# Kernel tuning notes

Hardware: AMD Instinct MI355X
Metric: run time of the kernel (lower is better)

## Reference

```python
import jax, jax.numpy as jnp
import numpy as np

NI, ND, NH = 64, 64, 4
NB, NLOC, NNEI = 4, 2048, 64


def setup_inputs() -> dict:
    key = jax.random.key(0)
    ks = jax.random.split(key, 7)
    g1 = jax.random.normal(ks[0], (NB, NLOC, NI), dtype=jnp.float32)
    gg1 = jax.random.normal(ks[1], (NB, NLOC, NNEI, NI), dtype=jnp.float32)
    nlist_mask = jax.random.randint(ks[2], (NB, NLOC, NNEI), 0, 2).astype(bool)
    # torch Linear weight (out, in); store transposed for x @ W
    Wq = jax.random.normal(ks[3], (NI, ND * NH), dtype=jnp.float32) * (1.0 / np.sqrt(NI))
    Wkv = jax.random.normal(ks[4], (NI, (ND + NI) * NH), dtype=jnp.float32) * (1.0 / np.sqrt(NI))
    Wh = jax.random.normal(ks[5], (NI * NH, NI), dtype=jnp.float32) * (1.0 / np.sqrt(NI * NH))
    bh = jax.random.normal(ks[6], (NI,), dtype=jnp.float32) * 0.01
    return {"g1": g1, "gg1": gg1, "nlist_mask": nlist_mask,
            "Wq": Wq, "Wkv": Wkv, "Wh": Wh, "bh": bh}


def reference(g1, gg1, nlist_mask, Wq, Wkv, Wh, bh):
    nb, nloc, nnei = nlist_mask.shape
    ni, nd, nh = NI, ND, NH
    # q: (nb, nloc, nh, nd)
    q = (g1 @ Wq).reshape(nb, nloc, nd, nh).transpose(0, 1, 3, 2)
    # kv: (nb, nloc, nnei, nd, 2*nh) -> (nb, nloc, 2*nh, nnei, nd); valid since ni == nd
    kv = (gg1 @ Wkv).reshape(nb, nloc, nnei, nd, 2 * nh).transpose(0, 1, 4, 2, 3)
    k = kv[:, :, :nh]          # (nb, nloc, nh, nnei, nd)
    v = kv[:, :, nh:2 * nh]    # (nb, nloc, nh, nnei, nd)
    attnw = jnp.einsum('blhd,blhjd->blhj', q, k) / np.sqrt(nd).astype(np.float32)
    m = nlist_mask[:, :, None, :]  # (nb, nloc, 1, nnei)
    attnw = jnp.where(m, attnw, -jnp.inf)
    attnw = jax.nn.softmax(attnw, axis=-1)
    attnw = jnp.where(m, attnw, 0.0)
    ret = jnp.einsum('blhj,blhjd->blhd', attnw, v).reshape(nb, nloc, nh * ni)
    return ret @ Wh + bh
```

## Files before the change

### kernel.cpp

```cpp
#include <hip/hip_runtime.h>
#include <hip/hip_fp16.h>
#include <math.h>

#define NATOM 8192

namespace {

typedef _Float16 half8 __attribute__((ext_vector_type(8)));
typedef _Float16 half2t __attribute__((ext_vector_type(2)));
typedef float f32x4 __attribute__((ext_vector_type(4)));

constexpr int VB_STRIDE = 260;

__global__ void pack_weights(const float* __restrict__ Wkv,
                             const float* __restrict__ Wq,
                             const float* __restrict__ Wh,
                             _Float16* __restrict__ out) {
  int tid = blockIdx.x * 256 + threadIdx.x;
  if (tid < 32768) {
    int i = tid >> 9, c = tid & 511;
    int ks = i >> 5, jj = i & 7, lq = (i >> 3) & 3;
    int ct = c >> 4, lr = c & 15;
    int l = lq * 16 + lr;
    out[(((ct * 2 + ks) * 64) + l) * 8 + jj] = (_Float16)Wkv[i * 512 + c];
  } else if (tid < 49152) {
    int idx = tid - 32768;
    int i = idx >> 8, c = idx & 255;
    out[32768 + c * 64 + i] = (_Float16)Wq[i * 256 + c];
  } else {
    int idx = tid - 49152;
    int k = idx >> 6, c = idx & 63;
    out[49152 + c * 256 + k] = (_Float16)Wh[k * 64 + c];
  }
}

__device__ __forceinline__ float dot8(half8 a, half8 b, float acc) {
  acc = __builtin_amdgcn_fdot2((half2t){a[0], a[1]}, (half2t){b[0], b[1]}, acc, false);
  acc = __builtin_amdgcn_fdot2((half2t){a[2], a[3]}, (half2t){b[2], b[3]}, acc, false);
  acc = __builtin_amdgcn_fdot2((half2t){a[4], a[5]}, (half2t){b[4], b[5]}, acc, false);
  acc = __builtin_amdgcn_fdot2((half2t){a[6], a[7]}, (half2t){b[6], b[7]}, acc, false);
  return acc;
}

__global__ __launch_bounds__(256, 4)
void local_atten_kernel(const float* __restrict__ g1,
                        const float* __restrict__ gg1,
                        const int* __restrict__ mask,
                        const _Float16* __restrict__ wpack,
                        const float* __restrict__ bh,
                        float* __restrict__ out) {
  __shared__ __align__(16) __half vraw[64 * VB_STRIDE];
  __shared__ __align__(16) __half g1h[64];
  __shared__ __align__(16) unsigned char blob[3072];
  __shared__ __align__(8) __half aws2[64][4];
  __shared__ __align__(16) __half rets[256];

  float* qs = reinterpret_cast<float*>(blob);
  __half (*sred)[4][64] = reinterpret_cast<__half(*)[4][64]>(blob + 1024);
  __half (*redbuf2)[64][4] = reinterpret_cast<__half(*)[64][4]>(blob);
  float (*redbuf)[64] = reinterpret_cast<float(*)[64]>(blob + 2048);

  const _Float16* wkvp = wpack;
  const _Float16* wqp  = wpack + 32768;
  const _Float16* whp  = wpack + 49152;

  const int t = threadIdx.x;
  const int lane = t & 63;
  const int wave = t >> 6;
  const int lq = lane >> 4;
  const int lr = lane & 15;
  const int atom = blockIdx.x;

  __half* gs = vraw;
  auto vbuf = reinterpret_cast<__half(*)[VB_STRIDE]>(vraw);

  const int mreg = mask[(size_t)atom * 64 + lane];
  const float bhv = bh[lane];
  if (t < 64) g1h[t] = __float2half(g1[(size_t)atom * 64 + t]);

  {
    const float4* src = reinterpret_cast<const float4*>(gg1 + (size_t)atom * 4096);
#pragma unroll
    for (int r = 0; r < 4; ++r) {
      int idx4 = t + 256 * r;
      int j = idx4 >> 4;
      int i4 = (idx4 & 15) << 2;
      float4 v = src[idx4];
      __half2 h01 = __floats2half2_rn(v.x, v.y);
      __half2 h23 = __floats2half2_rn(v.z, v.w);
      int g = i4 >> 3;
      int addr = j * 64 + ((g ^ (j & 7)) << 3) + (i4 & 7);
      union { __half2 h[2]; uint2 u; } pk;
      pk.h[0] = h01; pk.h[1] = h23;
      *reinterpret_cast<uint2*>(&gs[addr]) = pk.u;
    }
  }
  __syncthreads();

  half8 bfrag[4][2];
#pragma unroll
  for (int jt = 0; jt < 4; ++jt) {
#pragma unroll
    for (int ks = 0; ks < 2; ++ks) {
      int j = jt * 16 + lr;
      int g = ks * 4 + lq;
      bfrag[jt][ks] =
          *reinterpret_cast<const half8*>(&gs[j * 64 + ((g ^ (j & 7)) << 3)]);
    }
  }

  const half8* ap_base = reinterpret_cast<const half8*>(wkvp);
  half8 a0 = ap_base[(wave * 4) * 128 + lane];
  half8 a1 = ap_base[(wave * 4) * 128 + 64 + lane];

  {
    float qacc = 0.f;
    const half8* wrow = reinterpret_cast<const half8*>(wqp + t * 64);
    const half8* grow = reinterpret_cast<const half8*>(&g1h[0]);
#pragma unroll
    for (int ks = 0; ks < 8; ++ks) qacc = dot8(wrow[ks], grow[ks], qacc);
    qs[t] = qacc;
  }
  __syncthreads();

  float sacc[4][4];
#pragma unroll
  for (int jt = 0; jt < 4; ++jt)
#pragma unroll
    for (int h = 0; h < 4; ++h) sacc[jt][h] = 0.f;

  const bool isv = (lq & 1);
#pragma unroll
  for (int it = 0; it < 8; ++it) {
    const int ct = ((it >> 2) << 4) + wave * 4 + (it & 3);
    const int d = ct * 2 + (lq >> 1);

    half8 na0 = a0, na1 = a1;
    if (it < 7) {
      const int nit = it + 1;
      const int nct = ((nit >> 2) << 4) + wave * 4 + (nit & 3);
      na0 = ap_base[nct * 128 + lane];
      na1 = ap_base[nct * 128 + 64 + lane];
    }

    f32x4 accs[4];
#pragma unroll
    for (int jt = 0; jt < 4; ++jt) {
      f32x4 acc = {0.f, 0.f, 0.f, 0.f};
      acc = __builtin_amdgcn_mfma_f32_16x16x32_f16(a0, bfrag[jt][0], acc, 0, 0, 0);
      acc = __builtin_amdgcn_mfma_f32_16x16x32_f16(a1, bfrag[jt][1], acc, 0, 0, 0);
      accs[jt] = acc;
    }

    if (isv) {
#pragma unroll
      for (int jt = 0; jt < 4; ++jt) {
        int j = jt * 16 + lr;
        __half2 h01 = __floats2half2_rn(accs[jt][0], accs[jt][1]);
        __half2 h23 = __floats2half2_rn(accs[jt][2], accs[jt][3]);
        union { __half2 h[2]; uint2 u; } pk;
        pk.h[0] = h01; pk.h[1] = h23;
        *reinterpret_cast<uint2*>(&vbuf[j][d * 4]) = pk.u;
      }
    } else {
      float4 q4 = *reinterpret_cast<const float4*>(&qs[d * 4]);
#pragma unroll
      for (int jt = 0; jt < 4; ++jt) {
        sacc[jt][0] = fmaf(accs[jt][0], q4.x, sacc[jt][0]);
        sacc[jt][1] = fmaf(accs[jt][1], q4.y, sacc[jt][1]);
        sacc[jt][2] = fmaf(accs[jt][2], q4.z, sacc[jt][2]);
        sacc[jt][3] = fmaf(accs[jt][3], q4.w, sacc[jt][3]);
      }
    }
    a0 = na0; a1 = na1;
  }

#pragma unroll
  for (int jt = 0; jt < 4; ++jt)
#pragma unroll
    for (int h = 0; h < 4; ++h)
      sacc[jt][h] += __shfl_xor(sacc[jt][h], 32);
  if (lq == 0) {
#pragma unroll
    for (int h = 0; h < 4; ++h)
#pragma unroll
      for (int jt = 0; jt < 4; ++jt)
        sred[wave][h][jt * 16 + lr] = __float2half(sacc[jt][h]);
  }
  __syncthreads();

  half8 wh_frag[8];
  {
    const half8* wrow = reinterpret_cast<const half8*>(whp + lane * 256 + wave * 64);
#pragma unroll
    for (int ks = 0; ks < 8; ++ks) wh_frag[ks] = wrow[ks];
  }

  {
    float s = __half2float(sred[0][wave][lane]) + __half2float(sred[1][wave][lane]) +
              __half2float(sred[2][wave][lane]) + __half2float(sred[3][wave][lane]);
    s *= 0.125f;
    s = mreg ? s : -INFINITY;
    float mx = s;
#pragma unroll
    for (int off = 32; off > 0; off >>= 1) mx = fmaxf(mx, __shfl_xor(mx, off));
    float pe = mreg ? __expf(s - mx) : 0.f;
    float sum = pe;
#pragma unroll
    for (int off = 32; off > 0; off >>= 1) sum += __shfl_xor(sum, off);
    float aw = (sum > 0.f) ? (pe / sum) : 0.f;
    aws2[lane][wave] = __float2half(aw);
  }
  __syncthreads();

  {
    __half2 o01 = __float2half2_rn(0.f), o23 = __float2half2_rn(0.f);
#pragma unroll
    for (int jj = 0; jj < 16; ++jj) {
      int j = wave * 16 + jj;
      union { uint2 u; __half2 h[2]; } aw, vv;
      aw.u = *reinterpret_cast<const uint2*>(&aws2[j][0]);
      vv.u = *reinterpret_cast<const uint2*>(&vbuf[j][lane * 4]);
      o01 = __hfma2(aw.h[0], vv.h[0], o01);
      o23 = __hfma2(aw.h[1], vv.h[1], o23);
    }
    union { uint2 u; __half2 h[2]; } pk;
    pk.h[0] = o01; pk.h[1] = o23;
    *reinterpret_cast<uint2*>(&redbuf2[wave][lane][0]) = pk.u;
  }
  __syncthreads();

  {
    float r = 0.f;
#pragma unroll
    for (int jq = 0; jq < 4; ++jq) r += __half2float(redbuf2[jq][lane][wave]);
    rets[wave * 64 + lane] = __float2half(r);
  }

  {
    float part = 0.f;
    const half8* rrow = reinterpret_cast<const half8*>(&rets[wave * 64]);
#pragma unroll
    for (int ks = 0; ks < 8; ++ks) part = dot8(wh_frag[ks], rrow[ks], part);
    redbuf[wave][lane] = part;
  }
  __syncthreads();
  if (t < 64)
    out[(size_t)atom * 64 + t] =
        redbuf[0][t] + redbuf[1][t] + redbuf[2][t] + redbuf[3][t] + bhv;
}

}

extern "C" void kernel_launch(void* const* d_in, const int* in_sizes, int n_in,
                              void* d_out, int out_size, void* d_ws, size_t ws_size,
                              hipStream_t stream) {
  const float* g1   = (const float*)d_in[0];
  const float* gg1  = (const float*)d_in[1];
  const int*   mask = (const int*)d_in[2];
  const float* Wq   = (const float*)d_in[3];
  const float* Wkv  = (const float*)d_in[4];
  const float* Wh   = (const float*)d_in[5];
  const float* bh   = (const float*)d_in[6];
  float* out = (float*)d_out;
  (void)in_sizes; (void)n_in; (void)ws_size; (void)out_size;

  _Float16* wpack = (_Float16*)d_ws;
  pack_weights<<<256, 256, 0, stream>>>(Wkv, Wq, Wh, wpack);
  local_atten_kernel<<<NATOM, 256, 0, stream>>>(g1, gg1, mask, wpack, bh, out);
}
```

Before: 269.5 us.

## Drop weight-packing kernel and read fp32 weights directly in main kernel

Removes the separate pack_weights launch and has the attention kernel load the fp32 Wkv, Wq and Wh straight from global memory, converting Wkv to half in registers before the MFMAs. The q and output projections now use scalar fp32 FMA loops over shared inputs instead of packed-half dot products. This saves one kernel launch and the packing pass. In exchange, every block does strided scalar weight loads (16 per lane per iteration for Wkv) and extra conversions, which may raise memory traffic and register pressure.

```diff
diff --git a/kernel.cpp b/kernel.cpp
--- a/kernel.cpp
+++ b/kernel.cpp
@@ -7,62 +7,29 @@
 namespace {
 
 typedef _Float16 half8 __attribute__((ext_vector_type(8)));
-typedef _Float16 half2t __attribute__((ext_vector_type(2)));
 typedef float f32x4 __attribute__((ext_vector_type(4)));
 
 constexpr int VB_STRIDE = 260;
-
-__global__ void pack_weights(const float* __restrict__ Wkv,
-                             const float* __restrict__ Wq,
-                             const float* __restrict__ Wh,
-                             _Float16* __restrict__ out) {
-  int tid = blockIdx.x * 256 + threadIdx.x;
-  if (tid < 32768) {
-    int i = tid >> 9, c = tid & 511;
-    int ks = i >> 5, jj = i & 7, lq = (i >> 3) & 3;
-    int ct = c >> 4, lr = c & 15;
-    int l = lq * 16 + lr;
-    out[(((ct * 2 + ks) * 64) + l) * 8 + jj] = (_Float16)Wkv[i * 512 + c];
-  } else if (tid < 49152) {
-    int idx = tid - 32768;
-    int i = idx >> 8, c = idx & 255;
-    out[32768 + c * 64 + i] = (_Float16)Wq[i * 256 + c];
-  } else {
-    int idx = tid - 49152;
-    int k = idx >> 6, c = idx & 63;
-    out[49152 + c * 256 + k] = (_Float16)Wh[k * 64 + c];
-  }
-}
-
-__device__ __forceinline__ float dot8(half8 a, half8 b, float acc) {
-  acc = __builtin_amdgcn_fdot2((half2t){a[0], a[1]}, (half2t){b[0], b[1]}, acc, false);
-  acc = __builtin_amdgcn_fdot2((half2t){a[2], a[3]}, (half2t){b[2], b[3]}, acc, false);
-  acc = __builtin_amdgcn_fdot2((half2t){a[4], a[5]}, (half2t){b[4], b[5]}, acc, false);
-  acc = __builtin_amdgcn_fdot2((half2t){a[6], a[7]}, (half2t){b[6], b[7]}, acc, false);
-  return acc;
-}
 
 __global__ __launch_bounds__(256, 4)
 void local_atten_kernel(const float* __restrict__ g1,
                         const float* __restrict__ gg1,
                         const int* __restrict__ mask,
-                        const _Float16* __restrict__ wpack,
+                        const float* __restrict__ Wq,
+                        const float* __restrict__ Wkv,
+                        const float* __restrict__ Wh,
                         const float* __restrict__ bh,
                         float* __restrict__ out) {
   __shared__ __align__(16) __half vraw[64 * VB_STRIDE];
-  __shared__ __align__(16) __half g1h[64];
+  __shared__ __align__(16) float g1s[64];
   __shared__ __align__(16) unsigned char blob[3072];
   __shared__ __align__(8) __half aws2[64][4];
-  __shared__ __align__(16) __half rets[256];
+  __shared__ __align__(16) float rets[256];
 
   float* qs = reinterpret_cast<float*>(blob);
   __half (*sred)[4][64] = reinterpret_cast<__half(*)[4][64]>(blob + 1024);
   __half (*redbuf2)[64][4] = reinterpret_cast<__half(*)[64][4]>(blob);
   float (*redbuf)[64] = reinterpret_cast<float(*)[64]>(blob + 2048);
-
-  const _Float16* wkvp = wpack;
-  const _Float16* wqp  = wpack + 32768;
-  const _Float16* whp  = wpack + 49152;
 
   const int t = threadIdx.x;
   const int lane = t & 63;
@@ -76,7 +43,7 @@
 
   const int mreg = mask[(size_t)atom * 64 + lane];
   const float bhv = bh[lane];
-  if (t < 64) g1h[t] = __float2half(g1[(size_t)atom * 64 + t]);
+  if (t < 64) g1s[t] = g1[(size_t)atom * 64 + t];
 
   {
     const float4* src = reinterpret_cast<const float4*>(gg1 + (size_t)atom * 4096);
@@ -109,16 +76,22 @@
     }
   }
 
-  const half8* ap_base = reinterpret_cast<const half8*>(wkvp);
-  half8 a0 = ap_base[(wave * 4) * 128 + lane];
-  half8 a1 = ap_base[(wave * 4) * 128 + 64 + lane];
+  const float* wbase = Wkv + (size_t)(lq * 8) * 512 + lr;
+
+  float fcur[16];
+  {
+    const float* p = wbase + (wave * 4) * 16;
+#pragma unroll
+    for (int jj = 0; jj < 8; ++jj) {
+      fcur[jj]     = p[jj * 512];
+      fcur[8 + jj] = p[jj * 512 + 32 * 512];
+    }
+  }
 
   {
     float qacc = 0.f;
-    const half8* wrow = reinterpret_cast<const half8*>(wqp + t * 64);
-    const half8* grow = reinterpret_cast<const half8*>(&g1h[0]);
-#pragma unroll
-    for (int ks = 0; ks < 8; ++ks) qacc = dot8(wrow[ks], grow[ks], qacc);
+#pragma unroll 8
+    for (int i = 0; i < 64; ++i) qacc = fmaf(g1s[i], Wq[i * 256 + t], qacc);
     qs[t] = qacc;
   }
   __syncthreads();
@@ -135,12 +108,26 @@
     const int ct = ((it >> 2) << 4) + wave * 4 + (it & 3);
     const int d = ct * 2 + (lq >> 1);
 
-    half8 na0 = a0, na1 = a1;
+    half8 a0, a1;
+#pragma unroll
+    for (int jj = 0; jj < 8; ++jj) {
+      a0[jj] = (_Float16)fcur[jj];
+      a1[jj] = (_Float16)fcur[8 + jj];
+    }
+
+    float fnext[16];
     if (it < 7) {
       const int nit = it + 1;
       const int nct = ((nit >> 2) << 4) + wave * 4 + (nit & 3);
-      na0 = ap_base[nct * 128 + lane];
-      na1 = ap_base[nct * 128 + 64 + lane];
+      const float* p = wbase + nct * 16;
+#pragma unroll
+      for (int jj = 0; jj < 8; ++jj) {
+        fnext[jj]     = p[jj * 512];
+        fnext[8 + jj] = p[jj * 512 + 32 * 512];
+      }
+    } else {
+#pragma unroll
+      for (int jj = 0; jj < 16; ++jj) fnext[jj] = 0.f;
     }
 
     f32x4 accs[4];
@@ -172,7 +159,8 @@
         sacc[jt][3] = fmaf(accs[jt][3], q4.w, sacc[jt][3]);
       }
     }
-    a0 = na0; a1 = na1;
+#pragma unroll
+    for (int jj = 0; jj < 16; ++jj) fcur[jj] = fnext[jj];
   }
 
 #pragma unroll
@@ -188,13 +176,6 @@
         sred[wave][h][jt * 16 + lr] = __float2half(sacc[jt][h]);
   }
   __syncthreads();
-
-  half8 wh_frag[8];
-  {
-    const half8* wrow = reinterpret_cast<const half8*>(whp + lane * 256 + wave * 64);
-#pragma unroll
-    for (int ks = 0; ks < 8; ++ks) wh_frag[ks] = wrow[ks];
-  }
 
   {
     float s = __half2float(sred[0][wave][lane]) + __half2float(sred[1][wave][lane]) +
@@ -234,14 +215,14 @@
     float r = 0.f;
 #pragma unroll
     for (int jq = 0; jq < 4; ++jq) r += __half2float(redbuf2[jq][lane][wave]);
-    rets[wave * 64 + lane] = __float2half(r);
+    rets[wave * 64 + lane] = r;
   }
 
   {
     float part = 0.f;
-    const half8* rrow = reinterpret_cast<const half8*>(&rets[wave * 64]);
-#pragma unroll
-    for (int ks = 0; ks < 8; ++ks) part = dot8(wh_frag[ks], rrow[ks], part);
+#pragma unroll 8
+    for (int k = 0; k < 64; ++k)
+      part = fmaf(rets[wave * 64 + k], Wh[(wave * 64 + k) * 64 + lane], part);
     redbuf[wave][lane] = part;
   }
   __syncthreads();
@@ -263,9 +244,7 @@
   const float* Wh   = (const float*)d_in[5];
   const float* bh   = (const float*)d_in[6];
   float* out = (float*)d_out;
-  (void)in_sizes; (void)n_in; (void)ws_size; (void)out_size;
-
-  _Float16* wpack = (_Float16*)d_ws;
-  pack_weights<<<256, 256, 0, stream>>>(Wkv, Wq, Wh, wpack);
-  local_atten_kernel<<<NATOM, 256, 0, stream>>>(g1, gg1, mask, wpack, bh, out);
+  (void)in_sizes; (void)n_in; (void)d_ws; (void)ws_size; (void)out_size;
+
+  local_atten_kernel<<<NATOM, 256, 0, stream>>>(g1, gg1, mask, Wq, Wkv, Wh, bh, out);
 }
```

Result: slower. 289.0 us (+7.2%).
